# Kernel optimization log

Hardware: AMD Instinct MI355X
Metric: run time of the kernel (lower is better)

## Reference

```python
import jax, jax.numpy as jnp
import numpy as np

EPS = 1.1920929e-07  # float32 eps, matches torch.finfo(torch.float32).eps
QMAX = 127.0         # 2**(8-1)-1 for 8-bit symmetric quantization
NUM_HEADS = 12


def _round_ste(x):
    return x + jax.lax.stop_gradient(jnp.round(x) - x)


def _floor_ste(x):
    return x + jax.lax.stop_gradient(jnp.floor(x) - x)


def _act_quant(x):
    # per-tensor symmetric 8-bit (QuantAct + SymmetricQuantFunction)
    s = jax.lax.stop_gradient(jnp.maximum(jnp.max(jnp.abs(x)) / QMAX, EPS))
    return jnp.clip(_round_ste(x / s), -QMAX - 1.0, QMAX), s


def _weight_quant(w):
    # per-output-channel symmetric 8-bit (scale.view(-1,1) path in linear_quantize)
    s = jax.lax.stop_gradient(jnp.maximum(jnp.max(jnp.abs(w), axis=1) / QMAX, EPS))
    return jnp.clip(_round_ste(w / s[:, None]), -QMAX - 1.0, QMAX), s


def _fixedpoint_requant(pre_act, pre_s, z_s):
    # fixedpoint_mul: requantize int accumulator (value pre_act on scale pre_s)
    # onto scale z_s using a 31-bit mantissa/exponent decomposition (batch_frexp).
    def int_path(pa):
        z_int = jnp.round(pa / pre_s)
        ns = pre_s / z_s
        e = jnp.floor(jnp.log2(ns)) + 1.0          # frexp exponent: ns = m * 2**e, m in [0.5,1)
        m = jnp.floor(ns * jnp.exp2(-e) * 2.0 ** 31 + 0.5)  # ROUND_HALF_UP mantissa * 2**31
        out = jnp.round(z_int * m * jnp.exp2(e - 31.0))
        return jnp.clip(out, -QMAX - 1.0, QMAX)
    hard = jax.lax.stop_gradient(int_path(pre_act))
    soft = pre_act / z_s                            # STE backward: grad / z_scaling_factor
    return soft + jax.lax.stop_gradient(hard - soft)


def _int_softmax(x_int, sf, output_bit=8, n=15):
    # IntSoftmax (shiftmax) with int_exp_shift; x_int = logits / sf (integer-valued)
    x_int = x_int - jnp.max(x_int, axis=-1, keepdims=True)
    x_int = x_int + _floor_ste(x_int / 2.0) - _floor_ste(x_int / 16.0)
    x0 = jax.lax.stop_gradient(jnp.floor(-1.0 / sf))
    x_int = jnp.maximum(x_int, n * x0)
    q = _floor_ste(x_int / x0)
    r = x_int - x0 * q
    exp_int = jnp.clip(_floor_ste((r / 2.0 - x0) * jnp.exp2(n - q)), 0.0, None)
    esum = jnp.minimum(jnp.sum(exp_int, axis=-1, keepdims=True), 2.0 ** 31 - 1.0)
    factor = _floor_ste((2.0 ** 31 - 1.0) / esum)
    exp_int = _floor_ste(exp_int * factor / 2.0 ** (31 - output_bit + 1))
    return exp_int, 1.0 / 2.0 ** (output_bit - 1)


def setup_inputs() -> dict:
    key = jax.random.key(0)
    k1, k2, k3, k4, k5 = jax.random.split(key, 5)
    B, N, C = 8, 577, 768
    return {
        "x": jax.random.normal(k1, (B, N, C), dtype=jnp.float32),
        "w_qkv": jax.random.normal(k2, (3 * C, C), dtype=jnp.float32) * 0.02,
        "b_qkv": jax.random.normal(k3, (3 * C,), dtype=jnp.float32) * 0.01,
        "w_proj": jax.random.normal(k4, (C, C), dtype=jnp.float32) * 0.02,
        "b_proj": jax.random.normal(k5, (C,), dtype=jnp.float32) * 0.01,
    }


def reference(x, w_qkv, b_qkv, w_proj, b_proj):
    B, N, C = x.shape
    H = NUM_HEADS
    D = C // H
    # ---- quantize input activation and qkv weight, integer GEMM ----
    x_int, s_x = _act_quant(x)                         # [B,N,C] int-valued, scalar scale
    wq_int, s_wq = _weight_quant(w_qkv)                # [3C,C], per-channel scale [3C]
    acc_s = s_x * s_wq                                 # accumulator scale [3C]
    qkv_int = jnp.einsum('bnc,oc->bno', x_int, wq_int) + _round_ste(b_qkv / acc_s)
    qkv_f = qkv_int * acc_s                            # dequantized qkv [B,N,3C]
    # ---- requantize qkv to per-tensor 8-bit via fixed-point mul ----
    s_qkv = jax.lax.stop_gradient(jnp.maximum(jnp.max(jnp.abs(qkv_f)) / QMAX, EPS))
    qkv8 = _fixedpoint_requant(qkv_f, acc_s, s_qkv)    # int8-valued [B,N,3C]
    qkv8 = qkv8.reshape(B, N, 3, H, D).transpose(2, 0, 3, 1, 4)
    q, k, v = qkv8[0], qkv8[1], qkv8[2]                # each [B,H,N,D]
    # ---- integer attention logits; float scale carries head_dim**-0.5 ----
    attn_int = jnp.einsum('bhnd,bhmd->bhnm', q, k)
    s_attn = s_qkv * s_qkv * (D ** -0.5)
    sm_int, s_sm = _int_softmax(attn_int, s_attn)      # int probs on scale 1/128
    # ---- integer attn @ v ----
    ctx_int = jnp.einsum('bhnm,bhmd->bhnd', sm_int, v)
    ctx_f = (ctx_int * (s_sm * s_qkv)).transpose(0, 2, 1, 3).reshape(B, N, C)
    s_ctx = jax.lax.stop_gradient(jnp.maximum(jnp.max(jnp.abs(ctx_f)) / QMAX, EPS))
    ctx8 = _fixedpoint_requant(ctx_f, s_sm * s_qkv, s_ctx)
    # ---- quantized output projection ----
    wp_int, s_wp = _weight_quant(w_proj)
    out_s = s_ctx * s_wp
    out_int = jnp.einsum('bnc,oc->bno', ctx8, wp_int) + _round_ste(b_proj / out_s)
    return out_int * out_s
```

## Files before the change

### kernel.cpp

```cpp
#include <hip/hip_runtime.h>
#include <math.h>

#define BQ 8
#define SEQ 577
#define CH 768
#define NH 12
#define HD 64
#define M_ROWS (BQ * SEQ)
#define QKV_CH (3 * CH)
#define NX (M_ROWS * CH)
#define EPSF 1.1920929e-07f
#define F2P31 2147483648.0f

#define VT_ROW 640
#define P_STRIDE 664

typedef __attribute__((ext_vector_type(4))) int i32x4;
typedef struct __align__(16) { long x, y; } L2T;

__device__ __forceinline__ float softmax_e(int svr, int mxr, float x0, float nx0) {
  float xi = (float)(svr - mxr);
  xi = xi + floorf(xi * 0.5f) - floorf(xi * 0.0625f);
  xi = fmaxf(xi, nx0);
  float qd = floorf(xi / x0);
  float rr = xi - x0 * qd;
  int qi = (int)qd;
  float p2 = __int_as_float((142 - qi) << 23);
  float e = floorf((rr * 0.5f - x0) * p2);
  return fmaxf(e, 0.0f);
}

__device__ __forceinline__ void mfma_gemm_core_lds(
    const signed char* __restrict__ A, const signed char* __restrict__ Bm,
    signed char* As, signed char* Bs,
    int arow0, int bcol0, int w, int lane, i32x4 acc[4][4]) {
  int c = lane & 15, q = lane >> 4;
  int lr = lane >> 2;
  int ksb = (lane & 3) << 4;
  const signed char* Aw = As + ((w & 1) << 12);
  const signed char* Bw = Bs + ((w >> 1) << 12);
  for (int k0 = 0; k0 < CH; k0 += 64) {
#pragma unroll
    for (int u = 0; u < 2; ++u) {
      int row = (w << 5) + (u << 4) + lr;
      __builtin_amdgcn_global_load_lds(
          (const __attribute__((address_space(1))) void*)(A + (size_t)(arow0 + row) * CH + k0 + ksb),
          (__attribute__((address_space(3))) void*)(As + (w << 11) + (u << 10)),
          16, 0, 0);
      __builtin_amdgcn_global_load_lds(
          (const __attribute__((address_space(1))) void*)(Bm + (size_t)(bcol0 + row) * CH + k0 + ksb),
          (__attribute__((address_space(3))) void*)(Bs + (w << 11) + (u << 10)),
          16, 0, 0);
    }
    __syncthreads();
    L2T af[4], bf[4];
#pragma unroll
    for (int i = 0; i < 4; ++i)
      af[i] = *(const L2T*)(Aw + (((i << 4) + c) << 6) + (q << 4));
#pragma unroll
    for (int j = 0; j < 4; ++j)
      bf[j] = *(const L2T*)(Bw + (((j << 4) + c) << 6) + (q << 4));
#pragma unroll
    for (int i = 0; i < 4; ++i)
#pragma unroll
      for (int j = 0; j < 4; ++j) {
        acc[i][j] = __builtin_amdgcn_mfma_i32_16x16x32_i8(af[i].x, bf[j].x, acc[i][j], 0, 0, 0);
        acc[i][j] = __builtin_amdgcn_mfma_i32_16x16x32_i8(af[i].y, bf[j].y, acc[i][j], 0, 0, 0);
      }
    __syncthreads();
  }
}

__global__ __launch_bounds__(256) void k_prep(
    const float* __restrict__ x, const float* __restrict__ w_qkv,
    const float* __restrict__ w_proj,
    signed char* __restrict__ WQ8, float* __restrict__ SWQ,
    signed char* __restrict__ WP8, float* __restrict__ SWP,
    unsigned* __restrict__ gmax) {
  __shared__ float red[4];
  int blk = blockIdx.x, tid = threadIdx.x;
  if (blk < QKV_CH + CH) {
    const float* wr; signed char* w8; float* sw; int r;
    if (blk < QKV_CH) { r = blk; wr = w_qkv + (size_t)r * CH; w8 = WQ8 + (size_t)r * CH; sw = SWQ; }
    else { r = blk - QKV_CH; wr = w_proj + (size_t)r * CH; w8 = WP8 + (size_t)r * CH; sw = SWP; }
    float m = 0.f;
    for (int c = tid; c < CH; c += 256) m = fmaxf(m, fabsf(wr[c]));
#pragma unroll
    for (int o = 32; o; o >>= 1) m = fmaxf(m, __shfl_xor(m, o, 64));
    if ((tid & 63) == 0) red[tid >> 6] = m;
    __syncthreads();
    float mm = fmaxf(fmaxf(red[0], red[1]), fmaxf(red[2], red[3]));
    float s = fmaxf(mm / 127.0f, EPSF);
    if (tid == 0) sw[r] = s;
    for (int c = tid; c < CH; c += 256) {
      float q = rintf(wr[c] / s);
      q = fminf(fmaxf(q, -128.f), 127.f);
      w8[c] = (signed char)q;
    }
  } else {
    int ab = blk - (QKV_CH + CH);
    float m = 0.f;
    for (int i = ab * 256 + tid; i < NX; i += 1024 * 256) m = fmaxf(m, fabsf(x[i]));
#pragma unroll
    for (int o = 32; o; o >>= 1) m = fmaxf(m, __shfl_xor(m, o, 64));
    if ((tid & 63) == 0) red[tid >> 6] = m;
    __syncthreads();
    if (tid == 0)
      atomicMax(gmax, __float_as_uint(fmaxf(fmaxf(red[0], red[1]), fmaxf(red[2], red[3]))));
  }
}

__global__ void k_aquant(const float* __restrict__ x, int n,
                         const unsigned* __restrict__ hdr, signed char* __restrict__ x8) {
  float s = fmaxf(__uint_as_float(hdr[0]) / 127.0f, EPSF);
  int stride = gridDim.x * blockDim.x;
  for (int i = blockIdx.x * blockDim.x + threadIdx.x; i < n; i += stride) {
    float q = rintf(x[i] / s);
    q = fminf(fmaxf(q, -128.f), 127.f);
    x8[i] = (signed char)q;
  }
}

__global__ __launch_bounds__(256) void k_gemm_qkv(
    const signed char* __restrict__ A, const signed char* __restrict__ Bm,
    const float* __restrict__ swq, const float* __restrict__ bias,
    const unsigned* __restrict__ hdr, int* __restrict__ Cq, unsigned* __restrict__ gq) {
  __shared__ signed char As[8192], Bs[8192];
  __shared__ float red[4];
  int t = threadIdx.x;
  int lane = t & 63, w = t >> 6;
  int c = lane & 15, q = lane >> 4;
  int arow = blockIdx.y * 128 + (w & 1) * 64;
  int bcol = blockIdx.x * 128 + (w >> 1) * 64;
  i32x4 acc[4][4] = {};
  mfma_gemm_core_lds(A, Bm, As, Bs, blockIdx.y * 128, blockIdx.x * 128, w, lane, acc);
  float s_x = fmaxf(__uint_as_float(hdr[0]) / 127.0f, EPSF);
  float lmax = 0.f;
#pragma unroll
  for (int j = 0; j < 4; ++j) {
    int ccol = bcol + j * 16 + c;
    float accs = s_x * swq[ccol];
    int bint = (int)rintf(bias[ccol] / accs);
#pragma unroll
    for (int i = 0; i < 4; ++i)
#pragma unroll
      for (int r = 0; r < 4; ++r) {
        int rr = arow + i * 16 + q * 4 + r;
        if (rr < M_ROWS) {
          int qv = acc[i][j][r] + bint;
          Cq[(size_t)rr * QKV_CH + ccol] = qv;
          lmax = fmaxf(lmax, fabsf((float)qv * accs));
        }
      }
  }
#pragma unroll
  for (int off = 32; off; off >>= 1) lmax = fmaxf(lmax, __shfl_xor(lmax, off, 64));
  if (lane == 0) red[w] = lmax;
  __syncthreads();
  if (t == 0)
    atomicMax(gq, __float_as_uint(fmaxf(fmaxf(red[0], red[1]), fmaxf(red[2], red[3]))));
}

#define QK_BLKS 870
__global__ __launch_bounds__(256) void k_qkv_requant(
    const int* __restrict__ Cq, const float* __restrict__ swq,
    const unsigned* __restrict__ hdr,
    signed char* __restrict__ Q8, signed char* __restrict__ K8,
    signed char* __restrict__ VT8) {
  float s_x = fmaxf(__uint_as_float(hdr[0]) / 127.0f, EPSF);
  float s_qkv = fmaxf(__uint_as_float(hdr[1]) / 127.0f, EPSF);
  int blk = blockIdx.x, tid = threadIdx.x;
  if (blk < QK_BLKS) {
    int bx = blk % 6, by = blk / 6;
    int o = bx * 256 + tid;
    float accs = s_x * swq[o];
    float ns = accs / s_qkv;
    int e; float f = frexpf(ns, &e);
    float mm = floorf(f * F2P31 + 0.5f);
    float pw = __int_as_float((e + 96) << 23);
    int isK = (o >= CH);
    int rem = o - (isK ? CH : 0);
    int h = rem >> 6, d = rem & 63;
    signed char* dstb = isK ? K8 : Q8;
    int bn0 = by * 32;
    int bnend = min(bn0 + 32, M_ROWS);
    for (int bn = bn0; bn < bnend; ++bn) {
      int qv = Cq[(size_t)bn * QKV_CH + o];
      float qf = (float)qv * accs;
      float z = rintf(qf / accs);
      float t8 = rintf((z * mm) * pw);
      t8 = fminf(fmaxf(t8, -128.f), 127.f);
      int b = bn / SEQ, n = bn - b * SEQ;
      dstb[(((size_t)(b * NH + h) * SEQ + n) << 6) + d] = (signed char)t8;
    }
  } else {
    __shared__ signed char VTt[64 * 68];
    int vt = blk - QK_BLKS;
    int bh = vt / 10, n0 = (vt - bh * 10) * 64;
    int b = bh / NH, h = bh - b * NH;
    int od = tid & 63;
    int o = 2 * CH + h * 64 + od;
    float accs = s_x * swq[o];
    float ns = accs / s_qkv;
    int e; float f = frexpf(ns, &e);
    float mm = floorf(f * F2P31 + 0.5f);
    float pw = __int_as_float((e + 96) << 23);
    int nr = tid >> 6;
    for (int p = 0; p < 16; ++p) {
      int nl = nr * 16 + p;
      int n = n0 + nl;
      signed char v = 0;
      if (n < SEQ) {
        int qv = Cq[(size_t)(b * SEQ + n) * QKV_CH + o];
        float qf = (float)qv * accs;
        float z = rintf(qf / accs);
        float t8 = rintf((z * mm) * pw);
        t8 = fminf(fmaxf(t8, -128.f), 127.f);
        v = (signed char)t8;
      }
      VTt[od * 68 + nl] = v;
    }
    __syncthreads();
    int w16 = tid & 15, dr = tid >> 4;
#pragma unroll
    for (int pp = 0; pp < 4; ++pp) {
      int d = pp * 16 + dr;
      int val = *(const int*)&VTt[d * 68 + w16 * 4];
      *(int*)(VT8 + (size_t)bh * (64 * VT_ROW) + (size_t)d * VT_ROW + n0 + w16 * 4) = val;
    }
  }
}

__global__ __launch_bounds__(256, 4) void k_attn(
    const signed char* __restrict__ Q8, const signed char* __restrict__ K8,
    const signed char* __restrict__ VT8, const unsigned* __restrict__ hdr,
    int* __restrict__ ctxi, unsigned* __restrict__ gctx) {
  __shared__ unsigned char P[16 * P_STRIDE];
  __shared__ int Rmax[4][16];
  __shared__ double Rsum[4][16];
  __shared__ float Rav[4];
  int tid = threadIdx.x;
  int t = tid & 63, wid = tid >> 6;
  int lin = blockIdx.x;
  int j = lin >> 3;
  int bh = (lin & 7) * 12 + j / 37;
  int qt = j % 37;
  int b = bh / NH, h = bh - b * NH;
  int col = t & 15, q4 = t >> 4;
  {
    int r = tid >> 4, w4 = tid & 15;
    *(int*)&P[r * P_STRIDE + 576 + (w4 << 2)] = 0;
  }
  const signed char* Qb = Q8 + (((size_t)bh * SEQ + qt * 16 + col) << 6);
  long qa0 = *(const long*)(Qb + q4 * 8);
  long qa1 = *(const long*)(Qb + 32 + q4 * 8);
  const signed char* Kb = K8 + ((size_t)bh * SEQ << 6);
  int kt0 = (wid == 0) ? 0 : 10 + (wid - 1) * 9;
  int ktn = (wid == 0) ? 10 : 9;
  i32x4 sv[10];
  int mx[4] = {-2147483647 - 1, -2147483647 - 1, -2147483647 - 1, -2147483647 - 1};
#pragma unroll
  for (int u = 0; u < 10; ++u) {
    if (u < ktn) {
      int kt = kt0 + u;
      const signed char* kr = Kb + ((size_t)(kt * 16 + col) << 6);
      long kb0 = *(const long*)(kr + q4 * 8);
      long kb1 = *(const long*)(kr + 32 + q4 * 8);
      i32x4 a = {0, 0, 0, 0};
      a = __builtin_amdgcn_mfma_i32_16x16x32_i8(qa0, kb0, a, 0, 0, 0);
      a = __builtin_amdgcn_mfma_i32_16x16x32_i8(qa1, kb1, a, 0, 0, 0);
      sv[u] = a;
      bool valid = (kt < 36) | (col < 1);
#pragma unroll
      for (int r = 0; r < 4; ++r)
        if (valid) mx[r] = max(mx[r], a[r]);
    }
  }
#pragma unroll
  for (int r = 0; r < 4; ++r) {
    mx[r] = max(mx[r], __shfl_xor(mx[r], 1, 64));
    mx[r] = max(mx[r], __shfl_xor(mx[r], 2, 64));
    mx[r] = max(mx[r], __shfl_xor(mx[r], 4, 64));
    mx[r] = max(mx[r], __shfl_xor(mx[r], 8, 64));
  }
  if (col == 0) {
#pragma unroll
    for (int r = 0; r < 4; ++r) Rmax[wid][q4 * 4 + r] = mx[r];
  }
  __syncthreads();
#pragma unroll
  for (int r = 0; r < 4; ++r) {
    int row = q4 * 4 + r;
    mx[r] = max(max(Rmax[0][row], Rmax[1][row]), max(Rmax[2][row], Rmax[3][row]));
  }
  float s_qkv = fmaxf(__uint_as_float(hdr[1]) / 127.0f, EPSF);
  float s_attn = (s_qkv * s_qkv) * 0.125f;
  float x0 = floorf(-1.0f / s_attn);
  float nx0 = 15.0f * x0;
  double ds[4] = {0.0, 0.0, 0.0, 0.0};
#pragma unroll
  for (int u = 0; u < 10; ++u) {
    if (u < ktn) {
      int kt = kt0 + u;
      bool valid = (kt < 36) | (col < 1);
#pragma unroll
      for (int r = 0; r < 4; ++r) {
        float e = softmax_e(sv[u][r], mx[r], x0, nx0);
        e = valid ? e : 0.0f;
        ds[r] += (double)e;
        sv[u][r] = __float_as_int(e);
      }
    }
  }
#pragma unroll
  for (int r = 0; r < 4; ++r) {
    ds[r] += __shfl_xor(ds[r], 1, 64);
    ds[r] += __shfl_xor(ds[r], 2, 64);
    ds[r] += __shfl_xor(ds[r], 4, 64);
    ds[r] += __shfl_xor(ds[r], 8, 64);
  }
  if (col == 0) {
#pragma unroll
    for (int r = 0; r < 4; ++r) Rsum[wid][q4 * 4 + r] = ds[r];
  }
  __syncthreads();
  float fac[4];
#pragma unroll
  for (int r = 0; r < 4; ++r) {
    int row = q4 * 4 + r;
    double d = ((Rsum[0][row] + Rsum[1][row]) + Rsum[2][row]) + Rsum[3][row];
    float esum = fminf((float)d, F2P31);
    fac[r] = floorf(F2P31 / esum);
  }
#pragma unroll
  for (int u = 0; u < 10; ++u) {
    if (u < ktn) {
      int kt = kt0 + u;
#pragma unroll
      for (int r = 0; r < 4; ++r) {
        float e = __int_as_float(sv[u][r]);
        int p = (int)floorf((e * fac[r]) * 5.9604644775390625e-08f);
        P[(q4 * 4 + r) * P_STRIDE + kt * 16 + col] = (unsigned char)p;
      }
    }
  }
  __syncthreads();
  const signed char* Vb = VT8 + (size_t)bh * (64 * VT_ROW);
  i32x4 acc = {0, 0, 0, 0};
  for (int mc = 0; mc < 20; ++mc) {
    long pa = *(const long*)&P[col * P_STRIDE + mc * 32 + q4 * 8];
    long vb = *(const long*)(Vb + (size_t)(wid * 16 + col) * VT_ROW + mc * 32 + q4 * 8);
    acc = __builtin_amdgcn_mfma_i32_16x16x32_i8(pa, vb, acc, 0, 0, 0);
  }
  float pre_s = 0.0078125f * s_qkv;
  float avmax = 0.f;
#pragma unroll
  for (int r = 0; r < 4; ++r) {
    int n = qt * 16 + q4 * 4 + r;
    if (n < SEQ) {
      int cacc = acc[r];
      ctxi[((size_t)(b * SEQ + n)) * CH + h * 64 + wid * 16 + col] = cacc;
      avmax = fmaxf(avmax, fabsf((float)cacc * pre_s));
    }
  }
#pragma unroll
  for (int off = 32; off; off >>= 1) avmax = fmaxf(avmax, __shfl_xor(avmax, off, 64));
  if (t == 0) Rav[wid] = avmax;
  __syncthreads();
  if (tid == 0)
    atomicMax(gctx, __float_as_uint(fmaxf(fmaxf(Rav[0], Rav[1]), fmaxf(Rav[2], Rav[3]))));
}

__global__ void k_ctx_requant(const int* __restrict__ ctxi, const unsigned* __restrict__ hdr,
                              signed char* __restrict__ C8) {
  float s_qkv = fmaxf(__uint_as_float(hdr[1]) / 127.0f, EPSF);
  float pre_s = 0.0078125f * s_qkv;
  float s_ctx = fmaxf(__uint_as_float(hdr[2]) / 127.0f, EPSF);
  float ns = pre_s / s_ctx;
  int e;
  float f = frexpf(ns, &e);
  float mm = floorf(f * F2P31 + 0.5f);
  float pw = exp2f((float)e - 31.0f);
  int total4 = (M_ROWS * CH) / 4;
  int stride = gridDim.x * blockDim.x;
  const int4* src = (const int4*)ctxi;
  int* dst = (int*)C8;
  for (int i = blockIdx.x * blockDim.x + threadIdx.x; i < total4; i += stride) {
    int4 v = src[i];
    int pk = 0;
#pragma unroll
    for (int u = 0; u < 4; ++u) {
      int cv = (u == 0) ? v.x : (u == 1) ? v.y : (u == 2) ? v.z : v.w;
      float cf = (float)cv * pre_s;
      float z = rintf(cf / pre_s);
      float t8 = rintf((z * mm) * pw);
      t8 = fminf(fmaxf(t8, -128.f), 127.f);
      pk |= ((int)(signed char)t8 & 0xff) << (u * 8);
    }
    dst[i] = pk;
  }
}

__global__ __launch_bounds__(256) void k_gemm_out(
    const signed char* __restrict__ A, const signed char* __restrict__ Bm,
    const float* __restrict__ swp, const float* __restrict__ bias,
    const unsigned* __restrict__ hdr, float* __restrict__ outp) {
  __shared__ signed char As[8192], Bs[8192];
  int t = threadIdx.x;
  int lane = t & 63, w = t >> 6;
  int c = lane & 15, q = lane >> 4;
  int arow = blockIdx.y * 128 + (w & 1) * 64;
  int bcol = blockIdx.x * 128 + (w >> 1) * 64;
  i32x4 acc[4][4] = {};
  mfma_gemm_core_lds(A, Bm, As, Bs, blockIdx.y * 128, blockIdx.x * 128, w, lane, acc);
  float s_ctx = fmaxf(__uint_as_float(hdr[2]) / 127.0f, EPSF);
#pragma unroll
  for (int j = 0; j < 4; ++j) {
    int ccol = bcol + j * 16 + c;
    float outs = s_ctx * swp[ccol];
    int bint = (int)rintf(bias[ccol] / outs);
#pragma unroll
    for (int i = 0; i < 4; ++i)
#pragma unroll
      for (int r = 0; r < 4; ++r) {
        int rr = arow + i * 16 + q * 4 + r;
        if (rr < M_ROWS)
          outp[(size_t)rr * CH + ccol] = (float)(acc[i][j][r] + bint) * outs;
      }
  }
}

extern "C" void kernel_launch(void* const* d_in, const int* in_sizes, int n_in,
                              void* d_out, int out_size, void* d_ws, size_t ws_size,
                              hipStream_t stream) {
  const float* x = (const float*)d_in[0];
  const float* w_qkv = (const float*)d_in[1];
  const float* b_qkv = (const float*)d_in[2];
  const float* w_proj = (const float*)d_in[3];
  const float* b_proj = (const float*)d_in[4];
  float* outp = (float*)d_out;

  char* ws = (char*)d_ws;
  size_t off = 0;
  auto alloc = [&](size_t sz) -> char* {
    char* p = ws + off;
    off = (off + sz + 4095) & ~(size_t)4095;
    return p;
  };
  unsigned* hdr = (unsigned*)alloc(256);
  float* SWQ = (float*)alloc(QKV_CH * 4);
  float* SWP = (float*)alloc(CH * 4);
  signed char* WQ8 = (signed char*)alloc((size_t)QKV_CH * CH);
  signed char* WP8 = (signed char*)alloc((size_t)CH * CH);
  signed char* X8  = (signed char*)alloc((size_t)(M_ROWS + 128) * CH);
  signed char* Q8  = (signed char*)alloc((size_t)M_ROWS * CH);
  signed char* K8  = (signed char*)alloc((size_t)M_ROWS * CH);
  signed char* VT8 = (signed char*)alloc((size_t)BQ * NH * 64 * VT_ROW);
  signed char* C8  = (signed char*)alloc((size_t)(M_ROWS + 128) * CH);
  int* QKVI = (int*)alloc((size_t)M_ROWS * QKV_CH * 4);
  int* CTXI = (int*)alloc((size_t)M_ROWS * CH * 4);
  (void)ws_size;

  hipMemsetAsync(hdr, 0, 256, stream);
  k_prep<<<QKV_CH + CH + 1024, 256, 0, stream>>>(x, w_qkv, w_proj, WQ8, SWQ, WP8, SWP, hdr + 0);
  k_aquant<<<2048, 256, 0, stream>>>(x, NX, hdr, X8);
  dim3 g1(QKV_CH / 128, (M_ROWS + 127) / 128);
  k_gemm_qkv<<<g1, 256, 0, stream>>>(X8, WQ8, SWQ, b_qkv, hdr, QKVI, hdr + 1);
  k_qkv_requant<<<QK_BLKS + BQ * NH * 10, 256, 0, stream>>>(QKVI, SWQ, hdr, Q8, K8, VT8);
  k_attn<<<37 * BQ * NH, 256, 0, stream>>>(Q8, K8, VT8, hdr, CTXI, hdr + 2);
  k_ctx_requant<<<1024, 256, 0, stream>>>(CTXI, hdr, C8);
  dim3 g2(CH / 128, (M_ROWS + 127) / 128);
  k_gemm_out<<<g2, 256, 0, stream>>>(C8, WP8, SWP, b_proj, hdr, outp);
}
```

Before: 225.3 us.

## Use integer shift-exp softmax and vectorize activation absmax and quantize

Replaces the float shiftmax exponent (floor divisions, float power-of-two construction, double accumulation) in the attention kernel with pure integer arithmetic: arithmetic shifts, a magic-number reciprocal for division by x0, and a shift for the power of two, with row sums accumulated in 64-bit integers. Separately, the activation absmax reduction and the int8 quantization kernel now load float4 and store four packed bytes per thread. These aim to cut ALU and FP64 cost in softmax and memory transactions in the quantize passes. Risks are exact bit-equivalence of the integer exp with the float reference for edge cases, and the quantize kernel assumes n is divisible by four.

```diff
diff --git a/kernel.cpp b/kernel.cpp
--- a/kernel.cpp
+++ b/kernel.cpp
@@ -17,18 +17,6 @@
 
 typedef __attribute__((ext_vector_type(4))) int i32x4;
 typedef struct __align__(16) { long x, y; } L2T;
-
-__device__ __forceinline__ float softmax_e(int svr, int mxr, float x0, float nx0) {
-  float xi = (float)(svr - mxr);
-  xi = xi + floorf(xi * 0.5f) - floorf(xi * 0.0625f);
-  xi = fmaxf(xi, nx0);
-  float qd = floorf(xi / x0);
-  float rr = xi - x0 * qd;
-  int qi = (int)qd;
-  float p2 = __int_as_float((142 - qi) << 23);
-  float e = floorf((rr * 0.5f - x0) * p2);
-  return fmaxf(e, 0.0f);
-}
 
 __device__ __forceinline__ void mfma_gemm_core_lds(
     const signed char* __restrict__ A, const signed char* __restrict__ Bm,
@@ -99,8 +87,12 @@
     }
   } else {
     int ab = blk - (QKV_CH + CH);
+    const float4* x4 = (const float4*)x;
     float m = 0.f;
-    for (int i = ab * 256 + tid; i < NX; i += 1024 * 256) m = fmaxf(m, fabsf(x[i]));
+    for (int i = ab * 256 + tid; i < NX / 4; i += 1024 * 256) {
+      float4 v = x4[i];
+      m = fmaxf(m, fmaxf(fmaxf(fabsf(v.x), fabsf(v.y)), fmaxf(fabsf(v.z), fabsf(v.w))));
+    }
 #pragma unroll
     for (int o = 32; o; o >>= 1) m = fmaxf(m, __shfl_xor(m, o, 64));
     if ((tid & 63) == 0) red[tid >> 6] = m;
@@ -113,11 +105,21 @@
 __global__ void k_aquant(const float* __restrict__ x, int n,
                          const unsigned* __restrict__ hdr, signed char* __restrict__ x8) {
   float s = fmaxf(__uint_as_float(hdr[0]) / 127.0f, EPSF);
+  int n4 = n >> 2;
+  const float4* x4 = (const float4*)x;
+  int* dst = (int*)x8;
   int stride = gridDim.x * blockDim.x;
-  for (int i = blockIdx.x * blockDim.x + threadIdx.x; i < n; i += stride) {
-    float q = rintf(x[i] / s);
-    q = fminf(fmaxf(q, -128.f), 127.f);
-    x8[i] = (signed char)q;
+  for (int i = blockIdx.x * blockDim.x + threadIdx.x; i < n4; i += stride) {
+    float4 v = x4[i];
+    int pk = 0;
+#pragma unroll
+    for (int u = 0; u < 4; ++u) {
+      float xv = (u == 0) ? v.x : (u == 1) ? v.y : (u == 2) ? v.z : v.w;
+      float q = rintf(xv / s);
+      q = fminf(fmaxf(q, -128.f), 127.f);
+      pk |= ((int)(signed char)q & 0xff) << (u * 8);
+    }
+    dst[i] = pk;
   }
 }
 
@@ -237,7 +239,7 @@
     int* __restrict__ ctxi, unsigned* __restrict__ gctx) {
   __shared__ unsigned char P[16 * P_STRIDE];
   __shared__ int Rmax[4][16];
-  __shared__ double Rsum[4][16];
+  __shared__ unsigned long long Rsum[4][16];
   __shared__ float Rav[4];
   int tid = threadIdx.x;
   int t = tid & 63, wid = tid >> 6;
@@ -295,9 +297,14 @@
   }
   float s_qkv = fmaxf(__uint_as_float(hdr[1]) / 127.0f, EPSF);
   float s_attn = (s_qkv * s_qkv) * 0.125f;
-  float x0 = floorf(-1.0f / s_attn);
-  float nx0 = 15.0f * x0;
-  double ds[4] = {0.0, 0.0, 0.0, 0.0};
+  float x0f = floorf(-1.0f / s_attn);
+  int x0i = (int)x0f;
+  int bi = -x0i;
+  int nx0i = 15 * x0i;
+  int twob = bi << 1;
+  unsigned Mq = 0xFFFFFFFFu / (unsigned)bi + 1u;
+  bool bOne = (Mq == 0u);
+  unsigned long long su[4] = {0ull, 0ull, 0ull, 0ull};
 #pragma unroll
   for (int u = 0; u < 10; ++u) {
     if (u < ktn) {
@@ -305,31 +312,39 @@
       bool valid = (kt < 36) | (col < 1);
 #pragma unroll
       for (int r = 0; r < 4; ++r) {
-        float e = softmax_e(sv[u][r], mx[r], x0, nx0);
-        e = valid ? e : 0.0f;
-        ds[r] += (double)e;
-        sv[u][r] = __float_as_int(e);
+        int d = sv[u][r] - mx[r];
+        int xi = d + (d >> 1) - (d >> 4);
+        xi = max(xi, nx0i);
+        xi = min(xi, 0);
+        unsigned a = (unsigned)(-xi);
+        unsigned q = bOne ? a : __umulhi(a, Mq);
+        int rr = (int)(a - q * (unsigned)bi);
+        unsigned m = (unsigned)(twob - rr);
+        unsigned ue = (q < 15u) ? (m << (14 - q)) : (m >> 1);
+        ue = valid ? ue : 0u;
+        su[r] += ue;
+        sv[u][r] = (int)ue;
       }
     }
   }
 #pragma unroll
   for (int r = 0; r < 4; ++r) {
-    ds[r] += __shfl_xor(ds[r], 1, 64);
-    ds[r] += __shfl_xor(ds[r], 2, 64);
-    ds[r] += __shfl_xor(ds[r], 4, 64);
-    ds[r] += __shfl_xor(ds[r], 8, 64);
+    su[r] += __shfl_xor(su[r], 1, 64);
+    su[r] += __shfl_xor(su[r], 2, 64);
+    su[r] += __shfl_xor(su[r], 4, 64);
+    su[r] += __shfl_xor(su[r], 8, 64);
   }
   if (col == 0) {
 #pragma unroll
-    for (int r = 0; r < 4; ++r) Rsum[wid][q4 * 4 + r] = ds[r];
+    for (int r = 0; r < 4; ++r) Rsum[wid][q4 * 4 + r] = su[r];
   }
   __syncthreads();
   float fac[4];
 #pragma unroll
   for (int r = 0; r < 4; ++r) {
     int row = q4 * 4 + r;
-    double d = ((Rsum[0][row] + Rsum[1][row]) + Rsum[2][row]) + Rsum[3][row];
-    float esum = fminf((float)d, F2P31);
+    unsigned long long dv = ((Rsum[0][row] + Rsum[1][row]) + Rsum[2][row]) + Rsum[3][row];
+    float esum = fminf((float)dv, F2P31);
     fac[r] = floorf(F2P31 / esum);
   }
 #pragma unroll
@@ -338,7 +353,7 @@
       int kt = kt0 + u;
 #pragma unroll
       for (int r = 0; r < 4; ++r) {
-        float e = __int_as_float(sv[u][r]);
+        float e = (float)(unsigned)sv[u][r];
         int p = (int)floorf((e * fac[r]) * 5.9604644775390625e-08f);
         P[(q4 * 4 + r) * P_STRIDE + kt * 16 + col] = (unsigned char)p;
       }
```

New measurement: 223.4 us. No clear change (-0.8%).
